# Kernel optimization log

Measured on AMD Instinct MI355X. Metric: run time of the kernel, lower is better.

## Reference

```python
import jax, jax.numpy as jnp
import numpy as np


def setup_inputs() -> dict:
    key = jax.random.key(0)
    ks = jax.random.split(key, 8)
    B, C, T, V = 64, 256, 64, 25
    h = 8
    x_cls = jax.random.normal(ks[0], (B, C, 1, V), dtype=jnp.float32)
    x_patch = jax.random.normal(ks[1], (B, C, T, V), dtype=jnp.float32)
    s = 0.02
    q_w = jax.random.normal(ks[2], (C, C), dtype=jnp.float32) * s
    k_w = jax.random.normal(ks[3], (C, C), dtype=jnp.float32) * s
    v_w = jax.random.normal(ks[4], (C, C), dtype=jnp.float32) * s
    temp = jnp.ones((h, 1), dtype=jnp.float32)
    proj_w = jax.random.normal(ks[5], (C, C), dtype=jnp.float32) * s
    proj_b = jnp.zeros((C,), dtype=jnp.float32)
    return {"x_cls": x_cls, "x_patch": x_patch, "q_w": q_w, "k_w": k_w,
            "v_w": v_w, "temp": temp, "proj_w": proj_w, "proj_b": proj_b}


def reference(x_cls, x_patch, q_w, k_w, v_w, temp, proj_w, proj_b):
    B, C, _, V = x_cls.shape
    T = x_patch.shape[2]
    h = temp.shape[0]
    hd = C // h
    # (B, C, 1, V) -> (B, V, C) token layout; patches -> (B, T*V, C)
    xc = jnp.transpose(x_cls.reshape(B, C, V), (0, 2, 1))
    xp = jnp.transpose(x_patch.reshape(B, C, T * V), (0, 2, 1))
    # nn.Linear: y = x @ W.T (no bias since qkv_bias=False)
    q = (xc @ q_w.T).reshape(B, V, h, hd).transpose(0, 2, 1, 3)        # (B,h,V,hd)
    k = (xp @ k_w.T).reshape(B, T * V, h, hd).transpose(0, 2, 1, 3)    # (B,h,TV,hd)
    v = (xp @ v_w.T).reshape(B, T * V, h, hd).transpose(0, 2, 1, 3)    # (B,h,TV,hd)
    # scores: (B,h,V,TV), scaled by 1/sqrt(hd) then per-head temperature
    scale = 1.0 / jnp.sqrt(jnp.asarray(hd, dtype=q.dtype))
    attn = jnp.einsum('bhqd,bhkd->bhqk', q, k) * scale
    attn = attn * temp[None, :, :, None]  # temp (h,1) -> broadcast (1,h,1,1)
    attn = jax.nn.softmax(attn, axis=-1)
    out = jnp.einsum('bhqk,bhkd->bhqd', attn, v)                       # (B,h,V,hd)
    out = out.transpose(0, 2, 1, 3).reshape(B, V, C)
    out = out @ proj_w.T + proj_b
    return jnp.transpose(out, (0, 2, 1)).reshape(B, C, 1, V)
```

## Files before the change

kernel.cpp:

```cpp
#include <hip/hip_runtime.h>

#define B_ 64
#define C_ 256
#define TV_ 1600
#define V_ 25
#define H_ 8

typedef __attribute__((ext_vector_type(2))) int   intx2;
typedef __attribute__((ext_vector_type(4))) int   intx4;
typedef __attribute__((ext_vector_type(4))) float floatx4;
typedef __attribute__((ext_vector_type(8))) short short8;

__device__ __forceinline__ unsigned short f2bf(float f) {
    union { float f; unsigned u; } c; c.f = f;
    unsigned u = c.u;
    u += 0x7fffu + ((u >> 16) & 1u);
    return (unsigned short)(u >> 16);
}
__device__ __forceinline__ float bf2f(unsigned short s) {
    union { unsigned u; float f; } c; c.u = ((unsigned)s) << 16;
    return c.f;
}
__device__ __forceinline__ int pk_bf2(float a, float b) {
    return (int)((unsigned)f2bf(a) | ((unsigned)f2bf(b) << 16));
}

__global__ __launch_bounds__(256) void kz_zero(float* __restrict__ zbase,
        const float* __restrict__ vw, const float* __restrict__ pw,
        unsigned short* __restrict__ VWB, unsigned short* __restrict__ PWB) {
    const int blk = blockIdx.x;
    if (blk < 528) {
        const int i = blk * 256 + threadIdx.x;
        ((floatx4*)zbase)[i] = (floatx4){0.f, 0.f, 0.f, 0.f};
    } else {
        const int g = (blk - 528) * 256 + threadIdx.x;
        const floatx4 v = ((const floatx4*)vw)[g];
        const floatx4 p = ((const floatx4*)pw)[g];
        ((intx2*)VWB)[g] = (intx2){pk_bf2(v[0], v[1]), pk_bf2(v[2], v[3])};
        ((intx2*)PWB)[g] = (intx2){pk_bf2(p[0], p[1]), pk_bf2(p[2], p[3])};
    }
}

__global__ __launch_bounds__(256) void k1_trans(const float* __restrict__ xp,
                                                unsigned short* __restrict__ XF) {
    __shared__ float xs[128 * 68];
    const int blk = blockIdx.x;
    const int b = blk / 25, nb = blk - b * 25;
    const int n0 = nb * 64;
    const int t = threadIdx.x;
    const int cl = t & 127, nh = (t >> 7) * 32;
    const int n = t & 63, cq = t >> 6;
    for (int p = 0; p < 2; p++) {
        const float* src = xp + ((size_t)(b * C_ + p * 128 + cl)) * TV_ + n0 + nh;
        floatx4 v[8];
        #pragma unroll
        for (int j = 0; j < 8; j++) v[j] = *(const floatx4*)(src + 4 * j);
        if (p) __syncthreads();
        #pragma unroll
        for (int j = 0; j < 8; j++) *(floatx4*)&xs[cl * 68 + nh + 4 * j] = v[j];
        __syncthreads();
        #pragma unroll
        for (int j4 = 0; j4 < 4; j4++) {
            const int cgl = cq * 4 + j4, c8 = cgl * 8;
            intx4 w;
            w[0] = pk_bf2(xs[(c8 + 0) * 68 + n], xs[(c8 + 1) * 68 + n]);
            w[1] = pk_bf2(xs[(c8 + 2) * 68 + n], xs[(c8 + 3) * 68 + n]);
            w[2] = pk_bf2(xs[(c8 + 4) * 68 + n], xs[(c8 + 5) * 68 + n]);
            w[3] = pk_bf2(xs[(c8 + 6) * 68 + n], xs[(c8 + 7) * 68 + n]);
            const size_t chunk = (size_t)(b * 50 + nb * 2 + (n >> 5)) * 1024
                               + (p * 16 + cgl) * 32 + (n & 31);
            *(intx4*)(XF + chunk * 8) = w;
        }
        if (!p) __syncthreads();
    }
}

__global__ __launch_bounds__(256) void k0_qtilde(const float* __restrict__ xcls,
        const float* __restrict__ qw, const float* __restrict__ kw,
        const float* __restrict__ temp, unsigned short* __restrict__ QT) {
    __shared__ float xq[25 * 260];
    __shared__ float qh[25 * 33];
    __shared__ float kws[32 * 264];
    const int blk = blockIdx.x;
    const int b = blk >> 3, h = blk & 7;
    const int t = threadIdx.x;
    {
        const float* src = xcls + ((size_t)(b * C_ + t)) * V_;
        #pragma unroll
        for (int q = 0; q < V_; q++) xq[q * 260 + t] = src[q];
    }
    {
        const int d = t >> 3, c0 = (t & 7) * 32;
        const float* src = kw + (size_t)(h * 32 + d) * C_ + c0;
        #pragma unroll
        for (int j4 = 0; j4 < 8; j4++)
            *(floatx4*)&kws[d * 264 + c0 + 4 * j4] = *(const floatx4*)(src + 4 * j4);
    }
    __syncthreads();
    for (int idx = t; idx < 800; idx += 256) {
        const int q = idx >> 5, d = idx & 31;
        const float* qwr = qw + (size_t)(h * 32 + d) * C_;
        float acc = 0.f;
        for (int c4 = 0; c4 < 64; c4++) {
            const floatx4 a = *(const floatx4*)(qwr + 4 * c4);
            const floatx4 x = *(const floatx4*)&xq[q * 260 + 4 * c4];
            acc += a[0] * x[0] + a[1] * x[1] + a[2] * x[2] + a[3] * x[3];
        }
        qh[q * 33 + d] = acc;
    }
    __syncthreads();
    const float scale = temp[h] * 0.17677669529663689f * 1.4426950408889634f;
    const int qp = t & 31, cg = t >> 5;
    const int c0 = cg * 32;
    if (qp < 25) {
        floatx4 a4[8];
        #pragma unroll
        for (int j = 0; j < 8; j++) a4[j] = (floatx4){0.f, 0.f, 0.f, 0.f};
        for (int d = 0; d < 32; d++) {
            const float a = qh[qp * 33 + d];
            #pragma unroll
            for (int j4 = 0; j4 < 8; j4++) {
                const floatx4 k4 = *(const floatx4*)&kws[d * 264 + c0 + 4 * j4];
                a4[j4][0] += a * k4[0]; a4[j4][1] += a * k4[1];
                a4[j4][2] += a * k4[2]; a4[j4][3] += a * k4[3];
            }
        }
        unsigned short* dst = QT + ((size_t)((b * H_ + h) * 25 + qp)) * C_ + c0;
        #pragma unroll
        for (int j8 = 0; j8 < 4; j8++) {
            intx4 w;
            w[0] = pk_bf2(scale * a4[j8 * 2][0],     scale * a4[j8 * 2][1]);
            w[1] = pk_bf2(scale * a4[j8 * 2][2],     scale * a4[j8 * 2][3]);
            w[2] = pk_bf2(scale * a4[j8 * 2 + 1][0], scale * a4[j8 * 2 + 1][1]);
            w[3] = pk_bf2(scale * a4[j8 * 2 + 1][2], scale * a4[j8 * 2 + 1][3]);
            *(intx4*)(dst + j8 * 8) = w;
        }
    }
}

__global__ __launch_bounds__(512, 2) void k2_attn(
        const unsigned short* __restrict__ XF, const unsigned short* __restrict__ QT,
        const unsigned short* __restrict__ VWB, float* __restrict__ OA,
        float* __restrict__ L) {
    __shared__ unsigned short Xs[8192];
    __shared__ unsigned short Ps[8][32 * 40];
    __shared__ unsigned short Vs[8][32 * 40];

    const int blk = blockIdx.x;
    const int b = blk & 63, s = blk >> 6;
    const int tid = threadIdx.x;
    const int h = tid >> 6;
    const int lane = tid & 63;
    const int quad = lane >> 4, l16 = lane & 15;

    short8 qf[2][8];
    {
        const unsigned short* qb = QT + (size_t)(b * H_ + h) * 25 * C_;
        #pragma unroll
        for (int mt = 0; mt < 2; mt++)
            #pragma unroll
            for (int ks = 0; ks < 8; ks++)
                qf[mt][ks] = *(const short8*)(qb + (mt * 16 + l16) * C_ + ks * 32 + quad * 8);
    }
    short8 vwf[2][8];
    #pragma unroll
    for (int dt = 0; dt < 2; dt++)
        #pragma unroll
        for (int ks = 0; ks < 8; ks++)
            vwf[dt][ks] = *(const short8*)(VWB + (size_t)(h * 32 + dt * 16 + l16) * C_ + ks * 32 + quad * 8);

    floatx4 oc[2][2];
    #pragma unroll
    for (int mt = 0; mt < 2; mt++)
        #pragma unroll
        for (int dt = 0; dt < 2; dt++) oc[mt][dt] = (floatx4){0.f, 0.f, 0.f, 0.f};
    float lsum[2][4];
    #pragma unroll
    for (int mt = 0; mt < 2; mt++)
        #pragma unroll
        for (int r = 0; r < 4; r++) lsum[mt][r] = 0.f;

    const unsigned short* xf_base = XF + (size_t)(b * 50 + s * 5) * 1024 * 8;
    intx4 px0 = *(const intx4*)(xf_base + (size_t)(tid * 2 + 0) * 8);
    intx4 px1 = *(const intx4*)(xf_base + (size_t)(tid * 2 + 1) * 8);

    for (int ti = 0; ti < 5; ti++) {
        *(intx4*)&Xs[(tid * 2 + 0) * 8] = px0;
        *(intx4*)&Xs[(tid * 2 + 1) * 8] = px1;
        __syncthreads();
        if (ti < 4) {
            const unsigned short* nxt = xf_base + (size_t)(ti + 1) * 1024 * 8;
            px0 = *(const intx4*)(nxt + (size_t)(tid * 2 + 0) * 8);
            px1 = *(const intx4*)(nxt + (size_t)(tid * 2 + 1) * 8);
        }
        floatx4 sc[2][2], va[2][2];
        #pragma unroll
        for (int i = 0; i < 2; i++)
            #pragma unroll
            for (int j = 0; j < 2; j++) {
                sc[i][j] = (floatx4){0.f, 0.f, 0.f, 0.f};
                va[i][j] = (floatx4){0.f, 0.f, 0.f, 0.f};
            }
        #pragma unroll
        for (int ks = 0; ks < 8; ks++) {
            const short8 xf0 = *(const short8*)&Xs[(((ks * 4 + quad) * 32) + l16) * 8];
            const short8 xf1 = *(const short8*)&Xs[(((ks * 4 + quad) * 32) + 16 + l16) * 8];
            sc[0][0] = __builtin_amdgcn_mfma_f32_16x16x32_bf16(qf[0][ks], xf0, sc[0][0], 0, 0, 0);
            sc[0][1] = __builtin_amdgcn_mfma_f32_16x16x32_bf16(qf[0][ks], xf1, sc[0][1], 0, 0, 0);
            sc[1][0] = __builtin_amdgcn_mfma_f32_16x16x32_bf16(qf[1][ks], xf0, sc[1][0], 0, 0, 0);
            sc[1][1] = __builtin_amdgcn_mfma_f32_16x16x32_bf16(qf[1][ks], xf1, sc[1][1], 0, 0, 0);
            va[0][0] = __builtin_amdgcn_mfma_f32_16x16x32_bf16(xf0, vwf[0][ks], va[0][0], 0, 0, 0);
            va[0][1] = __builtin_amdgcn_mfma_f32_16x16x32_bf16(xf0, vwf[1][ks], va[0][1], 0, 0, 0);
            va[1][0] = __builtin_amdgcn_mfma_f32_16x16x32_bf16(xf1, vwf[0][ks], va[1][0], 0, 0, 0);
            va[1][1] = __builtin_amdgcn_mfma_f32_16x16x32_bf16(xf1, vwf[1][ks], va[1][1], 0, 0, 0);
        }
        #pragma unroll
        for (int mt = 0; mt < 2; mt++)
            #pragma unroll
            for (int g = 0; g < 2; g++)
                #pragma unroll
                for (int r = 0; r < 4; r++) {
                    const float p = __builtin_amdgcn_exp2f(sc[mt][g][r]);
                    lsum[mt][r] += p;
                    Ps[h][(mt * 16 + quad * 4 + r) * 40 + g * 16 + l16] = f2bf(p);
                }
        #pragma unroll
        for (int g = 0; g < 2; g++)
            #pragma unroll
            for (int dt = 0; dt < 2; dt++)
                *(intx2*)&Vs[h][(dt * 16 + l16) * 40 + g * 16 + quad * 4] =
                    (intx2){pk_bf2(va[g][dt][0], va[g][dt][1]),
                            pk_bf2(va[g][dt][2], va[g][dt][3])};
        #pragma unroll
        for (int mt = 0; mt < 2; mt++) {
            const short8 pa = *(const short8*)&Ps[h][(mt * 16 + l16) * 40 + quad * 8];
            #pragma unroll
            for (int dt = 0; dt < 2; dt++) {
                const short8 vb = *(const short8*)&Vs[h][(dt * 16 + l16) * 40 + quad * 8];
                oc[mt][dt] = __builtin_amdgcn_mfma_f32_16x16x32_bf16(pa, vb, oc[mt][dt], 0, 0, 0);
            }
        }
        __syncthreads();
    }
    #pragma unroll
    for (int mt = 0; mt < 2; mt++)
        #pragma unroll
        for (int r = 0; r < 4; r++) {
            float v = lsum[mt][r];
            #pragma unroll
            for (int off = 1; off < 16; off <<= 1) v += __shfl_xor(v, off, 64);
            lsum[mt][r] = v;
        }
    const size_t bh = (size_t)(b * H_ + h);
    if (l16 == 0) {
        #pragma unroll
        for (int mt = 0; mt < 2; mt++)
            #pragma unroll
            for (int r = 0; r < 4; r++) {
                const int q = mt * 16 + quad * 4 + r;
                if (q < 25) atomicAdd(&L[bh * 32 + q], lsum[mt][r]);
            }
    }
    #pragma unroll
    for (int mt = 0; mt < 2; mt++)
        #pragma unroll
        for (int dt = 0; dt < 2; dt++)
            #pragma unroll
            for (int r = 0; r < 4; r++) {
                const int q = mt * 16 + quad * 4 + r;
                if (q < 25)
                    atomicAdd(&OA[bh * 1024 + q * 32 + dt * 16 + l16], oc[mt][dt][r]);
            }
}

__global__ __launch_bounds__(256) void k3_proj(const float* __restrict__ OA,
        const float* __restrict__ Lsum, const unsigned short* __restrict__ PWB,
        const float* __restrict__ pb, float* __restrict__ y) {
    __shared__ unsigned short OB[32 * 264];
    __shared__ float rl_s[256];
    const int blk = blockIdx.x;
    const int b = blk >> 1, i0 = (blk & 1) * 128;
    const int t = threadIdx.x;
    const int wv = t >> 6, lane = t & 63;
    const int quad = lane >> 4, l16 = lane & 15;
    {
        const int h = t >> 5, q = t & 31;
        const float lv = Lsum[(size_t)(b * H_ + h) * 32 + q];
        rl_s[t] = (q < 25) ? 1.0f / lv : 0.0f;
    }
    __syncthreads();
    for (int idx = t; idx < 8192; idx += 256) {
        const int q = idx >> 8, j = idx & 255;
        const int h2 = j >> 5, d = j & 31;
        const float val = (q < 25)
            ? OA[(size_t)(b * H_ + h2) * 1024 + q * 32 + d] * rl_s[h2 * 32 + q] : 0.f;
        OB[q * 264 + j] = f2bf(val);
    }
    __syncthreads();
    floatx4 oc[2][2];
    #pragma unroll
    for (int mt = 0; mt < 2; mt++)
        #pragma unroll
        for (int ntp = 0; ntp < 2; ntp++) oc[mt][ntp] = (floatx4){0.f, 0.f, 0.f, 0.f};
    #pragma unroll
    for (int ks = 0; ks < 8; ks++) {
        const short8 a0 = *(const short8*)&OB[l16 * 264 + ks * 32 + quad * 8];
        const short8 a1 = *(const short8*)&OB[(16 + l16) * 264 + ks * 32 + quad * 8];
        #pragma unroll
        for (int ntp = 0; ntp < 2; ntp++) {
            const int i = i0 + (wv * 2 + ntp) * 16 + l16;
            const short8 bv = *(const short8*)(PWB + (size_t)i * C_ + ks * 32 + quad * 8);
            oc[0][ntp] = __builtin_amdgcn_mfma_f32_16x16x32_bf16(a0, bv, oc[0][ntp], 0, 0, 0);
            oc[1][ntp] = __builtin_amdgcn_mfma_f32_16x16x32_bf16(a1, bv, oc[1][ntp], 0, 0, 0);
        }
    }
    #pragma unroll
    for (int ntp = 0; ntp < 2; ntp++) {
        const int i = i0 + (wv * 2 + ntp) * 16 + l16;
        const float bias = pb[i];
        #pragma unroll
        for (int mt = 0; mt < 2; mt++)
            #pragma unroll
            for (int r = 0; r < 4; r++) {
                const int q = mt * 16 + quad * 4 + r;
                if (q < 25) y[(size_t)b * 6400 + i * 25 + q] = oc[mt][ntp][r] + bias;
            }
    }
}

extern "C" void kernel_launch(void* const* d_in, const int* in_sizes, int n_in,
                              void* d_out, int out_size, void* d_ws, size_t ws_size,
                              hipStream_t stream) {
    const float* xcls = (const float*)d_in[0];
    const float* xp   = (const float*)d_in[1];
    const float* qw   = (const float*)d_in[2];
    const float* kw   = (const float*)d_in[3];
    const float* vw   = (const float*)d_in[4];
    const float* temp = (const float*)d_in[5];
    const float* pw   = (const float*)d_in[6];
    const float* pb   = (const float*)d_in[7];
    float* y = (float*)d_out;

    if (ws_size < (size_t)61415424) return;
    char* ws = (char*)d_ws;
    unsigned short* XF  = (unsigned short*)ws;
    unsigned short* QT  = (unsigned short*)(ws + 52428800);
    float*          OA  = (float*)(ws + 58990592);
    float*          L   = (float*)(ws + 61087744);
    unsigned short* VWB = (unsigned short*)(ws + 61153280);
    unsigned short* PWB = (unsigned short*)(ws + 61284352);

    hipLaunchKernelGGL(kz_zero,  dim3(592),  dim3(256), 0, stream, OA, vw, pw, VWB, PWB);
    hipLaunchKernelGGL(k1_trans, dim3(1600), dim3(256), 0, stream, xp, XF);
    hipLaunchKernelGGL(k0_qtilde,dim3(512),  dim3(256), 0, stream, xcls, qw, kw, temp, QT);
    hipLaunchKernelGGL(k2_attn,  dim3(640),  dim3(512), 0, stream, XF, QT, VWB, OA, L);
    hipLaunchKernelGGL(k3_proj,  dim3(128),  dim3(256), 0, stream, OA, L, PWB, pb, y);
}
```

Baseline: 299.4 us.

## Fuse patch transpose and bf16 conversion into attention kernel loads

Removes the separate transpose kernel that wrote a bf16 copy of x_patch into the workspace. The attention kernel now reads fp32 x_patch directly with strided 8-byte loads, converts to bf16 and packs into shared memory in the MFMA-friendly layout. This avoids writing and re-reading about 50 MB of intermediate data and saves one launch, at the cost of less coalesced global loads and extra conversion work inside the attention kernel. The launch bounds also ask for 4 blocks per CU instead of 2, which may force fewer registers per thread and cause spills.

```diff
diff --git a/kernel.cpp b/kernel.cpp
--- a/kernel.cpp
+++ b/kernel.cpp
@@ -8,6 +8,7 @@
 
 typedef __attribute__((ext_vector_type(2))) int   intx2;
 typedef __attribute__((ext_vector_type(4))) int   intx4;
+typedef __attribute__((ext_vector_type(2))) float floatx2;
 typedef __attribute__((ext_vector_type(4))) float floatx4;
 typedef __attribute__((ext_vector_type(8))) short short8;
 
@@ -41,40 +42,6 @@
     }
 }
 
-__global__ __launch_bounds__(256) void k1_trans(const float* __restrict__ xp,
-                                                unsigned short* __restrict__ XF) {
-    __shared__ float xs[128 * 68];
-    const int blk = blockIdx.x;
-    const int b = blk / 25, nb = blk - b * 25;
-    const int n0 = nb * 64;
-    const int t = threadIdx.x;
-    const int cl = t & 127, nh = (t >> 7) * 32;
-    const int n = t & 63, cq = t >> 6;
-    for (int p = 0; p < 2; p++) {
-        const float* src = xp + ((size_t)(b * C_ + p * 128 + cl)) * TV_ + n0 + nh;
-        floatx4 v[8];
-        #pragma unroll
-        for (int j = 0; j < 8; j++) v[j] = *(const floatx4*)(src + 4 * j);
-        if (p) __syncthreads();
-        #pragma unroll
-        for (int j = 0; j < 8; j++) *(floatx4*)&xs[cl * 68 + nh + 4 * j] = v[j];
-        __syncthreads();
-        #pragma unroll
-        for (int j4 = 0; j4 < 4; j4++) {
-            const int cgl = cq * 4 + j4, c8 = cgl * 8;
-            intx4 w;
-            w[0] = pk_bf2(xs[(c8 + 0) * 68 + n], xs[(c8 + 1) * 68 + n]);
-            w[1] = pk_bf2(xs[(c8 + 2) * 68 + n], xs[(c8 + 3) * 68 + n]);
-            w[2] = pk_bf2(xs[(c8 + 4) * 68 + n], xs[(c8 + 5) * 68 + n]);
-            w[3] = pk_bf2(xs[(c8 + 6) * 68 + n], xs[(c8 + 7) * 68 + n]);
-            const size_t chunk = (size_t)(b * 50 + nb * 2 + (n >> 5)) * 1024
-                               + (p * 16 + cgl) * 32 + (n & 31);
-            *(intx4*)(XF + chunk * 8) = w;
-        }
-        if (!p) __syncthreads();
-    }
-}
-
 __global__ __launch_bounds__(256) void k0_qtilde(const float* __restrict__ xcls,
         const float* __restrict__ qw, const float* __restrict__ kw,
         const float* __restrict__ temp, unsigned short* __restrict__ QT) {
@@ -138,8 +105,8 @@
     }
 }
 
-__global__ __launch_bounds__(512, 2) void k2_attn(
-        const unsigned short* __restrict__ XF, const unsigned short* __restrict__ QT,
+__global__ __launch_bounds__(512, 4) void k2_attn(
+        const float* __restrict__ xp, const unsigned short* __restrict__ QT,
         const unsigned short* __restrict__ VWB, float* __restrict__ OA,
         float* __restrict__ L) {
     __shared__ unsigned short Xs[8192];
@@ -152,6 +119,7 @@
     const int h = tid >> 6;
     const int lane = tid & 63;
     const int quad = lane >> 4, l16 = lane & 15;
+    const int cg = tid >> 4;
 
     short8 qf[2][8];
     {
@@ -180,18 +148,28 @@
         #pragma unroll
         for (int r = 0; r < 4; r++) lsum[mt][r] = 0.f;
 
-    const unsigned short* xf_base = XF + (size_t)(b * 50 + s * 5) * 1024 * 8;
-    intx4 px0 = *(const intx4*)(xf_base + (size_t)(tid * 2 + 0) * 8);
-    intx4 px1 = *(const intx4*)(xf_base + (size_t)(tid * 2 + 1) * 8);
+    const float* xp_b = xp + (size_t)b * C_ * TV_ + s * 160 + 2 * l16;
+    floatx2 pf[8];
+    #pragma unroll
+    for (int k = 0; k < 8; k++)
+        pf[k] = *(const floatx2*)(xp_b + (size_t)(cg * 8 + k) * TV_);
 
     for (int ti = 0; ti < 5; ti++) {
-        *(intx4*)&Xs[(tid * 2 + 0) * 8] = px0;
-        *(intx4*)&Xs[(tid * 2 + 1) * 8] = px1;
+        {
+            intx4 w0, w1;
+            w0[0] = pk_bf2(pf[0][0], pf[1][0]); w0[1] = pk_bf2(pf[2][0], pf[3][0]);
+            w0[2] = pk_bf2(pf[4][0], pf[5][0]); w0[3] = pk_bf2(pf[6][0], pf[7][0]);
+            w1[0] = pk_bf2(pf[0][1], pf[1][1]); w1[1] = pk_bf2(pf[2][1], pf[3][1]);
+            w1[2] = pk_bf2(pf[4][1], pf[5][1]); w1[3] = pk_bf2(pf[6][1], pf[7][1]);
+            *(intx4*)&Xs[(tid * 2 + 0) * 8] = w0;
+            *(intx4*)&Xs[(tid * 2 + 1) * 8] = w1;
+        }
         __syncthreads();
         if (ti < 4) {
-            const unsigned short* nxt = xf_base + (size_t)(ti + 1) * 1024 * 8;
-            px0 = *(const intx4*)(nxt + (size_t)(tid * 2 + 0) * 8);
-            px1 = *(const intx4*)(nxt + (size_t)(tid * 2 + 1) * 8);
+            const float* nxt = xp_b + (ti + 1) * 32;
+            #pragma unroll
+            for (int k = 0; k < 8; k++)
+                pf[k] = *(const floatx2*)(nxt + (size_t)(cg * 8 + k) * TV_);
         }
         floatx4 sc[2][2], va[2][2];
         #pragma unroll
@@ -341,18 +319,16 @@
     const float* pb   = (const float*)d_in[7];
     float* y = (float*)d_out;
 
-    if (ws_size < (size_t)61415424) return;
+    if (ws_size < (size_t)8986624) return;
     char* ws = (char*)d_ws;
-    unsigned short* XF  = (unsigned short*)ws;
-    unsigned short* QT  = (unsigned short*)(ws + 52428800);
-    float*          OA  = (float*)(ws + 58990592);
-    float*          L   = (float*)(ws + 61087744);
-    unsigned short* VWB = (unsigned short*)(ws + 61153280);
-    unsigned short* PWB = (unsigned short*)(ws + 61284352);
-
-    hipLaunchKernelGGL(kz_zero,  dim3(592),  dim3(256), 0, stream, OA, vw, pw, VWB, PWB);
-    hipLaunchKernelGGL(k1_trans, dim3(1600), dim3(256), 0, stream, xp, XF);
-    hipLaunchKernelGGL(k0_qtilde,dim3(512),  dim3(256), 0, stream, xcls, qw, kw, temp, QT);
-    hipLaunchKernelGGL(k2_attn,  dim3(640),  dim3(512), 0, stream, XF, QT, VWB, OA, L);
-    hipLaunchKernelGGL(k3_proj,  dim3(128),  dim3(256), 0, stream, OA, L, PWB, pb, y);
-}
+    unsigned short* QT  = (unsigned short*)ws;
+    float*          OA  = (float*)(ws + 6561792);
+    float*          L   = (float*)(ws + 8658944);
+    unsigned short* VWB = (unsigned short*)(ws + 8724480);
+    unsigned short* PWB = (unsigned short*)(ws + 8855552);
+
+    hipLaunchKernelGGL(kz_zero,  dim3(592), dim3(256), 0, stream, OA, vw, pw, VWB, PWB);
+    hipLaunchKernelGGL(k0_qtilde,dim3(512), dim3(256), 0, stream, xcls, qw, kw, temp, QT);
+    hipLaunchKernelGGL(k2_attn,  dim3(640), dim3(512), 0, stream, xp, QT, VWB, OA, L);
+    hipLaunchKernelGGL(k3_proj,  dim3(128), dim3(256), 0, stream, OA, L, PWB, pb, y);
+}
```

Result: slower. 371.5 us (+24.1%).
